# Optimization experiments

Measured on AMD Instinct MI355X. Metric: run time of the kernel, lower is better.

Reference implementation:

```python
import jax, jax.numpy as jnp
import numpy as np

N_NODES = 100000
N_EDGES = 1600000
IN_FEATS = 128
N_HIDDEN = 128
N_CLASSES = 40


def setup_inputs() -> dict:
    key = jax.random.key(0)
    ks = jax.random.split(key, 8)
    features = jax.random.normal(ks[0], (N_NODES, IN_FEATS), dtype=jnp.float32)
    src = jax.random.randint(ks[1], (N_EDGES,), 0, N_NODES, dtype=jnp.int32)
    dst = jax.random.randint(ks[2], (N_EDGES,), 0, N_NODES, dtype=jnp.int32)
    s = 1.0 / np.sqrt(N_HIDDEN)
    W1 = jax.random.normal(ks[3], (IN_FEATS, N_HIDDEN), dtype=jnp.float32) * s
    b1 = jnp.zeros((N_HIDDEN,), dtype=jnp.float32)
    W2 = jax.random.normal(ks[4], (N_HIDDEN, N_HIDDEN), dtype=jnp.float32) * s
    b2 = jnp.zeros((N_HIDDEN,), dtype=jnp.float32)
    W3 = jax.random.normal(ks[5], (N_HIDDEN, N_CLASSES), dtype=jnp.float32) * s
    b3 = jnp.zeros((N_CLASSES,), dtype=jnp.float32)
    return {"features": features, "src": src, "dst": dst,
            "W1": W1, "b1": b1, "W2": W2, "b2": b2, "W3": W3, "b3": b3}


def _gcn_layer(h, src, dst, W, b, activation):
    # message: copy src 'h' along edges; reduce: sum per dst node
    accum = jax.ops.segment_sum(h[src], dst, num_segments=N_NODES)  # [N, d]
    h = accum @ W + b
    if activation:
        h = jax.nn.relu(h)
    return h


def reference(features, src, dst, W1, b1, W2, b2, W3, b3):
    h = _gcn_layer(features, src, dst, W1, b1, True)
    h = _gcn_layer(h, src, dst, W2, b2, True)
    h = _gcn_layer(h, src, dst, W3, b3, False)
    return h  # [N_NODES, N_CLASSES]
```

## Files before the change

kernel.cpp:

```cpp
#include <hip/hip_runtime.h>
#include <hip/hip_bf16.h>


#define PBUCK  800
#define CAPB   4096

typedef __attribute__((ext_vector_type(8))) short short8;
typedef __attribute__((ext_vector_type(4))) float f32x4;

__device__ __forceinline__ float bflo(unsigned u) { return __uint_as_float(u << 16); }
__device__ __forceinline__ float bfhi(unsigned u) { return __uint_as_float(u & 0xffff0000u); }
__device__ __forceinline__ unsigned short f2bf(float f) {
    unsigned u = __float_as_uint(f);
    u = (u + 0x7fffu + ((u >> 16) & 1u)) >> 16;
    return (unsigned short)u;
}
__device__ __forceinline__ unsigned packbf(float a, float b) {
    return (unsigned)f2bf(a) | ((unsigned)f2bf(b) << 16);
}
__device__ __forceinline__ short8 as_short8(uint4 v) {
    union { uint4 u; short8 s; } x; x.u = v; return x.s;
}

__device__ __forceinline__ void packw_body(
    const float* __restrict__ W, unsigned short* __restrict__ Wp, int t)
{
    if (t >= 2048) return;
    int lane = t & 63, cg = (t >> 6) & 7, ks = t >> 9;
    int c = cg * 16 + (lane & 15);
    int kb = ks * 32 + (lane >> 4) * 8;
    unsigned short e[8];
    #pragma unroll
    for (int j = 0; j < 8; ++j) e[j] = f2bf(W[(size_t)(kb + j) * 128 + c]);
    uint4 v = make_uint4((unsigned)e[0] | ((unsigned)e[1] << 16),
                         (unsigned)e[2] | ((unsigned)e[3] << 16),
                         (unsigned)e[4] | ((unsigned)e[5] << 16),
                         (unsigned)e[6] | ((unsigned)e[7] << 16));
    *(uint4*)(Wp + (size_t)t * 8) = v;
}
__device__ __forceinline__ void packw3_body(
    const float* __restrict__ W, unsigned short* __restrict__ Wp, int t)
{
    if (t >= 768) return;
    int lane = t & 63, g = t >> 6;
    int ks = g / 3, cf = g % 3;
    int c = cf * 16 + (lane & 15);
    int kb = ks * 32 + (lane >> 4) * 8;
    unsigned short e[8];
    #pragma unroll
    for (int j = 0; j < 8; ++j)
        e[j] = (c < 40) ? f2bf(W[(size_t)(kb + j) * 40 + c]) : (unsigned short)0;
    uint4 v = make_uint4((unsigned)e[0] | ((unsigned)e[1] << 16),
                         (unsigned)e[2] | ((unsigned)e[3] << 16),
                         (unsigned)e[4] | ((unsigned)e[5] << 16),
                         (unsigned)e[6] | ((unsigned)e[7] << 16));
    *(uint4*)(Wp + (size_t)t * 8) = v;
}

__global__ __launch_bounds__(256) void setup_kernel(
    const float* __restrict__ feat, unsigned short* __restrict__ SC,
    const float* __restrict__ W1, const float* __restrict__ W2,
    const float* __restrict__ W3,
    unsigned short* __restrict__ Wp1, unsigned short* __restrict__ Wp2,
    unsigned short* __restrict__ Wp3, int* __restrict__ pcur,
    int* __restrict__ ghist, int* __restrict__ perm,
    int n_nodes, int castBlocks, int npad)
{
    int b = blockIdx.x, tid = threadIdx.x;
    if (b < castBlocks) {
        int i = b * 256 + tid;
        if (i < n_nodes * 16) {
            const float4* p = (const float4*)(feat + (size_t)i * 8);
            float4 a = p[0], bb = p[1];
            uint4 v = make_uint4(packbf(a.x, a.y), packbf(a.z, a.w),
                                 packbf(bb.x, bb.y), packbf(bb.z, bb.w));
            *(uint4*)(SC + (size_t)i * 8) = v;
        }
        return;
    }
    int r = b - castBlocks;
    if (r < 8)       packw_body(W1, Wp1, r * 256 + tid);
    else if (r < 16) packw_body(W2, Wp2, (r - 8) * 256 + tid);
    else if (r < 19) packw3_body(W3, Wp3, (r - 16) * 256 + tid);
    else if (r < 23) { int i = (r - 19) * 256 + tid; if (i < PBUCK) pcur[i] = i * CAPB; }
    else {
        if (tid < 128) ghist[tid] = 0;
        int idx = n_nodes + tid;
        if (idx < npad) perm[idx] = 0x7fffffff;
    }
}

__global__ __launch_bounds__(1024) void scatter_priv(
    const int* __restrict__ src, const int* __restrict__ dst,
    int* __restrict__ pcur, unsigned* __restrict__ rec, int n_edges)
{
    __shared__ int hist[PBUCK];
    __shared__ int base[PBUCK];
    int nb = gridDim.x;
    int chunk = (n_edges + nb - 1) / nb;
    int lo = blockIdx.x * chunk, hi = min(n_edges, lo + chunk);
    for (int i = threadIdx.x; i < PBUCK; i += 1024) hist[i] = 0;
    __syncthreads();
    for (int e = lo + threadIdx.x; e < hi; e += 1024)
        atomicAdd(&hist[dst[e] >> 7], 1);
    __syncthreads();
    for (int i = threadIdx.x; i < PBUCK; i += 1024) {
        int h = hist[i];
        base[i] = h ? atomicAdd(&pcur[i], h) : 0;
        hist[i] = 0;
    }
    __syncthreads();
    for (int e = lo + threadIdx.x; e < hi; e += 1024) {
        int d = dst[e];
        int b = d >> 7;
        int pos = base[b] + atomicAdd(&hist[b], 1);
        if (pos < (b + 1) * CAPB)
            rec[pos] = (unsigned)src[e] | ((unsigned)(d & 127) << 17);
    }
}

__global__ __launch_bounds__(512) void fill_local3(
    const unsigned* __restrict__ rec, const int* __restrict__ pcur,
    int* __restrict__ offs, int* __restrict__ esrc,
    int* __restrict__ ghist, int n_buckets, int n_nodes)
{
    __shared__ int cnt[128];
    __shared__ int cur[128];
    __shared__ int dh[128];
    __shared__ int wsum[8];
    __shared__ int redA[8], redL[8];
    const int b = blockIdx.x, tid = threadIdx.x;
    const int lane = tid & 63, wid = tid >> 6;

    int accL = 0, accA = 0;
    for (int i = tid; i < n_buckets; i += 512) {
        int t = min(pcur[i] - i * CAPB, CAPB);
        accA += t;
        if (i < b) accL += t;
    }
    #pragma unroll
    for (int off = 32; off; off >>= 1) {
        accA += __shfl_down(accA, off);
        accL += __shfl_down(accL, off);
    }
    if (lane == 0) { redA[wid] = accA; redL[wid] = accL; }
    if (tid < 128) { cnt[tid] = 0; dh[tid] = 0; }
    __syncthreads();
    int baseAll = 0, baseLt = 0;
    #pragma unroll
    for (int w = 0; w < 8; ++w) { baseAll += redA[w]; baseLt += redL[w]; }
    if (b == 0 && tid == 0) offs[n_nodes] = baseAll;

    const int node0 = b << 7;
    const int nN = min(128, n_nodes - node0);
    const int cbeg = b * CAPB;
    const int cend = cbeg + min(pcur[b] - cbeg, CAPB);

    for (int i = cbeg + tid; i < cend; i += 512)
        atomicAdd(&cnt[rec[i] >> 17], 1);
    __syncthreads();

    if (tid < nN) atomicAdd(&dh[min(cnt[tid], 127)], 1);
    int c = (tid < 128) ? cnt[tid] : 0;
    int incl = c;
    #pragma unroll
    for (int off = 1; off < 64; off <<= 1) { int q = __shfl_up(incl, off); if (lane >= off) incl += q; }
    if (lane == 63) wsum[wid] = incl;
    __syncthreads();
    int wpre = 0;
    for (int w = 0; w < wid; ++w) wpre += wsum[w];
    int excl = wpre + incl - c;
    if (tid < nN) { offs[node0 + tid] = baseLt + excl; cur[tid] = excl; }
    if (tid < 128 && dh[tid]) atomicAdd(&ghist[tid], dh[tid]);
    __syncthreads();

    for (int i = cbeg + tid; i < cend; i += 512) {
        unsigned r = rec[i];
        int pos = atomicAdd(&cur[r >> 17], 1);
        esrc[baseLt + pos] = (int)(r & 0x1FFFFu);
    }
}

__global__ __launch_bounds__(128) void deg_scan(
    const int* __restrict__ ghist, int* __restrict__ gcur)
{
    __shared__ int ws[2];
    int tid = threadIdx.x;
    int t = ghist[tid];
    int lane = tid & 63, wid = tid >> 6;
    int incl = t;
    #pragma unroll
    for (int off = 1; off < 64; off <<= 1) { int q = __shfl_up(incl, off); if (lane >= off) incl += q; }
    if (lane == 63) ws[wid] = incl;
    __syncthreads();
    int excl = (wid ? ws[0] : 0) + incl - t;
    gcur[tid] = excl;
}

__global__ __launch_bounds__(256) void deg_place(
    const int* __restrict__ offs, int* __restrict__ gcur,
    int* __restrict__ perm, int n_nodes)
{
    __shared__ int dh[128];
    __shared__ int dbase[128];
    int nb = gridDim.x;
    int chunk = (n_nodes + nb - 1) / nb;
    int lo = blockIdx.x * chunk, hi = min(n_nodes, lo + chunk);
    int tid = threadIdx.x;
    if (tid < 128) dh[tid] = 0;
    __syncthreads();
    for (int n = lo + tid; n < hi; n += 256) {
        int d = min(offs[n + 1] - offs[n], 127);
        atomicAdd(&dh[d], 1);
    }
    __syncthreads();
    if (tid < 128) {
        int h = dh[tid];
        dbase[tid] = h ? atomicAdd(&gcur[tid], h) : 0;
        dh[tid] = 0;
    }
    __syncthreads();
    for (int n = lo + tid; n < hi; n += 256) {
        int d = min(offs[n + 1] - offs[n], 127);
        int pos = dbase[d] + atomicAdd(&dh[d], 1);
        perm[pos] = n;
    }
}

#define GATHER128_BODY(hk, e, end)                                          \
    while (e < end && (e & 3)) {                                            \
        uint4 v = *(const uint4*)(hk + (size_t)esrc[e] * 128);              \
        a0 += bflo(v.x); a1 += bfhi(v.x); a2 += bflo(v.y); a3 += bfhi(v.y); \
        a4 += bflo(v.z); a5 += bfhi(v.z); a6 += bflo(v.w); a7 += bfhi(v.w); \
        ++e;                                                                \
    }                                                                       \
    for (; e + 3 < end; e += 4) {                                           \
        int4 ss = *(const int4*)(esrc + e);                                 \
        uint4 v0 = *(const uint4*)(hk + (size_t)ss.x * 128);                \
        uint4 v1 = *(const uint4*)(hk + (size_t)ss.y * 128);                \
        uint4 v2 = *(const uint4*)(hk + (size_t)ss.z * 128);                \
        uint4 v3 = *(const uint4*)(hk + (size_t)ss.w * 128);                \
        a0 += (bflo(v0.x) + bflo(v1.x)) + (bflo(v2.x) + bflo(v3.x));        \
        a1 += (bfhi(v0.x) + bfhi(v1.x)) + (bfhi(v2.x) + bfhi(v3.x));        \
        a2 += (bflo(v0.y) + bflo(v1.y)) + (bflo(v2.y) + bflo(v3.y));        \
        a3 += (bfhi(v0.y) + bfhi(v1.y)) + (bfhi(v2.y) + bfhi(v3.y));        \
        a4 += (bflo(v0.z) + bflo(v1.z)) + (bflo(v2.z) + bflo(v3.z));        \
        a5 += (bfhi(v0.z) + bfhi(v1.z)) + (bfhi(v2.z) + bfhi(v3.z));        \
        a6 += (bflo(v0.w) + bflo(v1.w)) + (bflo(v2.w) + bflo(v3.w));        \
        a7 += (bfhi(v0.w) + bfhi(v1.w)) + (bfhi(v2.w) + bfhi(v3.w));        \
    }                                                                       \
    for (; e < end; ++e) {                                                  \
        uint4 v = *(const uint4*)(hk + (size_t)esrc[e] * 128);              \
        a0 += bflo(v.x); a1 += bfhi(v.x); a2 += bflo(v.y); a3 += bfhi(v.y); \
        a4 += bflo(v.z); a5 += bfhi(v.z); a6 += bflo(v.w); a7 += bfhi(v.w); \
    }

__global__ __launch_bounds__(256, 8) void gather_gemm_f(
    const unsigned short* __restrict__ h, const int* __restrict__ offs,
    const int* __restrict__ esrc, const int* __restrict__ perm,
    const unsigned short* __restrict__ Wp, const float* __restrict__ bias,
    unsigned short* __restrict__ out, int n_nodes)
{
    __shared__ unsigned short accb[16 * 136];
    const int tid = threadIdx.x;
    const int nl = tid >> 4;
    const int k  = tid & 15;
    const int node0 = blockIdx.x * 16;
    const int node = perm[node0 + nl];

    float a0 = 0.f, a1 = 0.f, a2 = 0.f, a3 = 0.f;
    float a4 = 0.f, a5 = 0.f, a6 = 0.f, a7 = 0.f;
    if (node < n_nodes) {
        const unsigned short* hk = h + k * 8;
        int e = offs[node], end = offs[node + 1];
        GATHER128_BODY(hk, e, end)
    }
    {
        uint4 v = make_uint4(packbf(a0, a1), packbf(a2, a3),
                             packbf(a4, a5), packbf(a6, a7));
        *(uint4*)(accb + nl * 136 + k * 8) = v;
    }
    __syncthreads();

    const int w = tid >> 6, l = tid & 63;
    short8 afr[4];
    #pragma unroll
    for (int ks = 0; ks < 4; ++ks)
        afr[ks] = as_short8(*(const uint4*)(
            accb + (l & 15) * 136 + ks * 32 + (l >> 4) * 8));

    #pragma unroll
    for (int cf = 0; cf < 2; ++cf) {
        int cg = w * 2 + cf;
        int col = cg * 16 + (l & 15);
        float bb = bias[col];
        f32x4 vacc = { bb, bb, bb, bb };
        #pragma unroll
        for (int ks = 0; ks < 4; ++ks) {
            short8 bfr = as_short8(*(const uint4*)(Wp + (size_t)((ks * 8 + cg) * 64 + l) * 8));
            vacc = __builtin_amdgcn_mfma_f32_16x16x32_bf16(afr[ks], bfr, vacc, 0, 0, 0);
        }
        #pragma unroll
        for (int r = 0; r < 4; ++r) {
            int prow = perm[node0 + (l >> 4) * 4 + r];
            if (prow < n_nodes)
                out[(size_t)prow * 128 + col] = f2bf(fmaxf(vacc[r], 0.f));
        }
    }
}

__global__ __launch_bounds__(256, 8) void gather_gemm_ft(
    const unsigned short* __restrict__ h, const int* __restrict__ offs,
    const int* __restrict__ esrc, const int* __restrict__ perm,
    const unsigned short* __restrict__ Wp, const float* __restrict__ bias,
    const unsigned short* __restrict__ Wp3,
    unsigned short* __restrict__ tout, int n_nodes)
{
    __shared__ unsigned short accb[16 * 136];
    const int tid = threadIdx.x;
    const int nl = tid >> 4;
    const int k  = tid & 15;
    const int node0 = blockIdx.x * 16;
    const int node = perm[node0 + nl];

    float a0 = 0.f, a1 = 0.f, a2 = 0.f, a3 = 0.f;
    float a4 = 0.f, a5 = 0.f, a6 = 0.f, a7 = 0.f;
    if (node < n_nodes) {
        const unsigned short* hk = h + k * 8;
        int e = offs[node], end = offs[node + 1];
        GATHER128_BODY(hk, e, end)
    }
    {
        uint4 v = make_uint4(packbf(a0, a1), packbf(a2, a3),
                             packbf(a4, a5), packbf(a6, a7));
        *(uint4*)(accb + nl * 136 + k * 8) = v;
    }
    __syncthreads();

    const int w = tid >> 6, l = tid & 63;
    short8 afr[4];
    #pragma unroll
    for (int ks = 0; ks < 4; ++ks)
        afr[ks] = as_short8(*(const uint4*)(
            accb + (l & 15) * 136 + ks * 32 + (l >> 4) * 8));

    f32x4 hacc[2];
    #pragma unroll
    for (int cf = 0; cf < 2; ++cf) {
        int cg = w * 2 + cf;
        float bb = bias[cg * 16 + (l & 15)];
        f32x4 vacc = { bb, bb, bb, bb };
        #pragma unroll
        for (int ks = 0; ks < 4; ++ks) {
            short8 bfr = as_short8(*(const uint4*)(Wp + (size_t)((ks * 8 + cg) * 64 + l) * 8));
            vacc = __builtin_amdgcn_mfma_f32_16x16x32_bf16(afr[ks], bfr, vacc, 0, 0, 0);
        }
        hacc[cf] = vacc;
    }

    __syncthreads();
    #pragma unroll
    for (int cf = 0; cf < 2; ++cf) {
        int col = (w * 2 + cf) * 16 + (l & 15);
        #pragma unroll
        for (int r = 0; r < 4; ++r)
            accb[((l >> 4) * 4 + r) * 136 + col] = f2bf(fmaxf(hacc[cf][r], 0.f));
    }
    __syncthreads();

    if (w < 3) {
        short8 afr2[4];
        #pragma unroll
        for (int ks = 0; ks < 4; ++ks)
            afr2[ks] = as_short8(*(const uint4*)(
                accb + (l & 15) * 136 + ks * 32 + (l >> 4) * 8));
        f32x4 vacc = { 0.f, 0.f, 0.f, 0.f };
        #pragma unroll
        for (int ks = 0; ks < 4; ++ks) {
            short8 bfr = as_short8(*(const uint4*)(Wp3 + (size_t)((ks * 3 + w) * 64 + l) * 8));
            vacc = __builtin_amdgcn_mfma_f32_16x16x32_bf16(afr2[ks], bfr, vacc, 0, 0, 0);
        }
        int col = w * 16 + (l & 15);
        if (col < 40) {
            #pragma unroll
            for (int r = 0; r < 4; ++r) {
                int prow = perm[node0 + (l >> 4) * 4 + r];
                if (prow < n_nodes)
                    tout[(size_t)prow * 40 + col] = f2bf(vacc[r]);
            }
        }
    }
}

__global__ __launch_bounds__(256) void gather40v(
    const unsigned short* __restrict__ t, const int* __restrict__ offs,
    const int* __restrict__ esrc, const int* __restrict__ perm,
    const float* __restrict__ b3, float* __restrict__ out,
    int n_nodes, int npad)
{
    int lane = threadIdx.x & 63;
    int g = lane / 10;
    int k = lane - g * 10;
    int slot = blockIdx.x * 24 + (threadIdx.x >> 6) * 6 + g;
    if (g >= 6 || slot >= npad) return;
    int node = perm[slot];
    if (node >= n_nodes) return;
    float4 bv = *(const float4*)(b3 + k * 4);
    float a0 = bv.x, a1 = bv.y, a2 = bv.z, a3 = bv.w;
    int e = offs[node], end = offs[node + 1];
    while (e < end && (e & 3)) {
        uint2 v = *(const uint2*)(t + (size_t)esrc[e] * 40 + k * 4);
        a0 += bflo(v.x); a1 += bfhi(v.x); a2 += bflo(v.y); a3 += bfhi(v.y);
        ++e;
    }
    for (; e + 3 < end; e += 4) {
        int4 ss = *(const int4*)(esrc + e);
        uint2 v0 = *(const uint2*)(t + (size_t)ss.x * 40 + k * 4);
        uint2 v1 = *(const uint2*)(t + (size_t)ss.y * 40 + k * 4);
        uint2 v2 = *(const uint2*)(t + (size_t)ss.z * 40 + k * 4);
        uint2 v3 = *(const uint2*)(t + (size_t)ss.w * 40 + k * 4);
        a0 += (bflo(v0.x) + bflo(v1.x)) + (bflo(v2.x) + bflo(v3.x));
        a1 += (bfhi(v0.x) + bfhi(v1.x)) + (bfhi(v2.x) + bfhi(v3.x));
        a2 += (bflo(v0.y) + bflo(v1.y)) + (bflo(v2.y) + bflo(v3.y));
        a3 += (bfhi(v0.y) + bfhi(v1.y)) + (bfhi(v2.y) + bfhi(v3.y));
    }
    for (; e < end; ++e) {
        uint2 v = *(const uint2*)(t + (size_t)esrc[e] * 40 + k * 4);
        a0 += bflo(v.x); a1 += bfhi(v.x); a2 += bflo(v.y); a3 += bfhi(v.y);
    }
    *(float4*)(out + (size_t)node * 40 + k * 4) = make_float4(a0, a1, a2, a3);
}

extern "C" void kernel_launch(void* const* d_in, const int* in_sizes, int n_in,
                              void* d_out, int out_size, void* d_ws, size_t ws_size,
                              hipStream_t stream)
{
    const float* feat = (const float*)d_in[0];
    const int*   src  = (const int*)d_in[1];
    const int*   dst  = (const int*)d_in[2];
    const float* W1   = (const float*)d_in[3];
    const float* b1   = (const float*)d_in[4];
    const float* W2   = (const float*)d_in[5];
    const float* b2   = (const float*)d_in[6];
    const float* W3   = (const float*)d_in[7];
    const float* b3   = (const float*)d_in[8];
    float* out = (float*)d_out;

    const int n_edges = in_sizes[1];
    const int n_nodes = in_sizes[0] / 128;
    const int n_buckets = (n_nodes + 127) >> 7;
    const int fg = (n_nodes + 15) / 16;
    const int npad = fg * 16;

    unsigned short* SC = (unsigned short*)d_ws;
    unsigned short* SD = SC + (size_t)n_nodes * 128;
    unsigned* rec = (unsigned*)(SD + (size_t)n_nodes * 128);
    int*  esrc = (int*)(rec + (size_t)PBUCK * CAPB);
    int*  offs = esrc + n_edges;
    int*  pcur = offs + n_nodes + 1;
    unsigned short* Wp1 = (unsigned short*)(pcur + PBUCK);
    unsigned short* Wp2 = Wp1 + 2048 * 8;
    unsigned short* Wp3 = Wp2 + 2048 * 8;
    int* ghist = (int*)(Wp3 + 768 * 8);
    int* gcur  = ghist + 128;
    int* perm  = gcur + 128;

    const int castBlocks = (n_nodes * 16 + 255) / 256;

    setup_kernel<<<castBlocks + 24, 256, 0, stream>>>(
        feat, SC, W1, W2, W3, Wp1, Wp2, Wp3, pcur, ghist, perm,
        n_nodes, castBlocks, npad);
    scatter_priv<<<512, 1024, 0, stream>>>(src, dst, pcur, rec, n_edges);
    fill_local3<<<n_buckets, 512, 0, stream>>>(rec, pcur, offs, esrc, ghist,
                                               n_buckets, n_nodes);
    deg_scan<<<1, 128, 0, stream>>>(ghist, gcur);
    deg_place<<<256, 256, 0, stream>>>(offs, gcur, perm, n_nodes);

    gather_gemm_f<<<fg, 256, 0, stream>>>(SC, offs, esrc, perm, Wp1, b1, SD, n_nodes);

    gather_gemm_ft<<<fg, 256, 0, stream>>>(SD, offs, esrc, perm, Wp2, b2, Wp3, SC, n_nodes);

    gather40v<<<(npad + 23) / 24, 256, 0, stream>>>(SC, offs, esrc, perm, b3, out,
                                                    n_nodes, npad);
}
```

Before: 246.5 us.

## Drop degree-sorted node permutation and gather nodes in natural order

```diff
diff --git a/kernel.cpp b/kernel.cpp
--- a/kernel.cpp
+++ b/kernel.cpp
@@ -63,8 +63,7 @@
     const float* __restrict__ W3,
     unsigned short* __restrict__ Wp1, unsigned short* __restrict__ Wp2,
     unsigned short* __restrict__ Wp3, int* __restrict__ pcur,
-    int* __restrict__ ghist, int* __restrict__ perm,
-    int n_nodes, int castBlocks, int npad)
+    int n_nodes, int castBlocks)
 {
     int b = blockIdx.x, tid = threadIdx.x;
     if (b < castBlocks) {
@@ -82,12 +81,7 @@
     if (r < 8)       packw_body(W1, Wp1, r * 256 + tid);
     else if (r < 16) packw_body(W2, Wp2, (r - 8) * 256 + tid);
     else if (r < 19) packw3_body(W3, Wp3, (r - 16) * 256 + tid);
-    else if (r < 23) { int i = (r - 19) * 256 + tid; if (i < PBUCK) pcur[i] = i * CAPB; }
-    else {
-        if (tid < 128) ghist[tid] = 0;
-        int idx = n_nodes + tid;
-        if (idx < npad) perm[idx] = 0x7fffffff;
-    }
+    else { int i = (r - 19) * 256 + tid; if (i < PBUCK) pcur[i] = i * CAPB; }
 }
 
 __global__ __launch_bounds__(1024) void scatter_priv(
@@ -122,11 +116,10 @@
 __global__ __launch_bounds__(512) void fill_local3(
     const unsigned* __restrict__ rec, const int* __restrict__ pcur,
     int* __restrict__ offs, int* __restrict__ esrc,
-    int* __restrict__ ghist, int n_buckets, int n_nodes)
+    int n_buckets, int n_nodes)
 {
     __shared__ int cnt[128];
     __shared__ int cur[128];
-    __shared__ int dh[128];
     __shared__ int wsum[8];
     __shared__ int redA[8], redL[8];
     const int b = blockIdx.x, tid = threadIdx.x;
@@ -144,7 +137,7 @@
         accL += __shfl_down(accL, off);
     }
     if (lane == 0) { redA[wid] = accA; redL[wid] = accL; }
-    if (tid < 128) { cnt[tid] = 0; dh[tid] = 0; }
+    if (tid < 128) cnt[tid] = 0;
     __syncthreads();
     int baseAll = 0, baseLt = 0;
     #pragma unroll
@@ -160,7 +153,6 @@
         atomicAdd(&cnt[rec[i] >> 17], 1);
     __syncthreads();
 
-    if (tid < nN) atomicAdd(&dh[min(cnt[tid], 127)], 1);
     int c = (tid < 128) ? cnt[tid] : 0;
     int incl = c;
     #pragma unroll
@@ -171,59 +163,12 @@
     for (int w = 0; w < wid; ++w) wpre += wsum[w];
     int excl = wpre + incl - c;
     if (tid < nN) { offs[node0 + tid] = baseLt + excl; cur[tid] = excl; }
-    if (tid < 128 && dh[tid]) atomicAdd(&ghist[tid], dh[tid]);
     __syncthreads();
 
     for (int i = cbeg + tid; i < cend; i += 512) {
         unsigned r = rec[i];
         int pos = atomicAdd(&cur[r >> 17], 1);
         esrc[baseLt + pos] = (int)(r & 0x1FFFFu);
-    }
-}
-
-__global__ __launch_bounds__(128) void deg_scan(
-    const int* __restrict__ ghist, int* __restrict__ gcur)
-{
-    __shared__ int ws[2];
-    int tid = threadIdx.x;
-    int t = ghist[tid];
-    int lane = tid & 63, wid = tid >> 6;
-    int incl = t;
-    #pragma unroll
-    for (int off = 1; off < 64; off <<= 1) { int q = __shfl_up(incl, off); if (lane >= off) incl += q; }
-    if (lane == 63) ws[wid] = incl;
-    __syncthreads();
-    int excl = (wid ? ws[0] : 0) + incl - t;
-    gcur[tid] = excl;
-}
-
-__global__ __launch_bounds__(256) void deg_place(
-    const int* __restrict__ offs, int* __restrict__ gcur,
-    int* __restrict__ perm, int n_nodes)
-{
-    __shared__ int dh[128];
-    __shared__ int dbase[128];
-    int nb = gridDim.x;
-    int chunk = (n_nodes + nb - 1) / nb;
-    int lo = blockIdx.x * chunk, hi = min(n_nodes, lo + chunk);
-    int tid = threadIdx.x;
-    if (tid < 128) dh[tid] = 0;
-    __syncthreads();
-    for (int n = lo + tid; n < hi; n += 256) {
-        int d = min(offs[n + 1] - offs[n], 127);
-        atomicAdd(&dh[d], 1);
-    }
-    __syncthreads();
-    if (tid < 128) {
-        int h = dh[tid];
-        dbase[tid] = h ? atomicAdd(&gcur[tid], h) : 0;
-        dh[tid] = 0;
-    }
-    __syncthreads();
-    for (int n = lo + tid; n < hi; n += 256) {
-        int d = min(offs[n + 1] - offs[n], 127);
-        int pos = dbase[d] + atomicAdd(&dh[d], 1);
-        perm[pos] = n;
     }
 }
 
@@ -257,16 +202,15 @@
 
 __global__ __launch_bounds__(256, 8) void gather_gemm_f(
     const unsigned short* __restrict__ h, const int* __restrict__ offs,
-    const int* __restrict__ esrc, const int* __restrict__ perm,
-    const unsigned short* __restrict__ Wp, const float* __restrict__ bias,
-    unsigned short* __restrict__ out, int n_nodes)
+    const int* __restrict__ esrc, const unsigned short* __restrict__ Wp,
+    const float* __restrict__ bias, unsigned short* __restrict__ out,
+    int n_nodes)
 {
     __shared__ unsigned short accb[16 * 136];
     const int tid = threadIdx.x;
     const int nl = tid >> 4;
     const int k  = tid & 15;
-    const int node0 = blockIdx.x * 16;
-    const int node = perm[node0 + nl];
+    const int node = blockIdx.x * 16 + nl;
 
     float a0 = 0.f, a1 = 0.f, a2 = 0.f, a3 = 0.f;
     float a4 = 0.f, a5 = 0.f, a6 = 0.f, a7 = 0.f;
@@ -289,6 +233,7 @@
         afr[ks] = as_short8(*(const uint4*)(
             accb + (l & 15) * 136 + ks * 32 + (l >> 4) * 8));
 
+    const int node0 = blockIdx.x * 16;
     #pragma unroll
     for (int cf = 0; cf < 2; ++cf) {
         int cg = w * 2 + cf;
@@ -302,26 +247,24 @@
         }
         #pragma unroll
         for (int r = 0; r < 4; ++r) {
-            int prow = perm[node0 + (l >> 4) * 4 + r];
-            if (prow < n_nodes)
-                out[(size_t)prow * 128 + col] = f2bf(fmaxf(vacc[r], 0.f));
+            int row = node0 + (l >> 4) * 4 + r;
+            if (row < n_nodes)
+                out[(size_t)row * 128 + col] = f2bf(fmaxf(vacc[r], 0.f));
         }
     }
 }
 
 __global__ __launch_bounds__(256, 8) void gather_gemm_ft(
     const unsigned short* __restrict__ h, const int* __restrict__ offs,
-    const int* __restrict__ esrc, const int* __restrict__ perm,
-    const unsigned short* __restrict__ Wp, const float* __restrict__ bias,
-    const unsigned short* __restrict__ Wp3,
+    const int* __restrict__ esrc, const unsigned short* __restrict__ Wp,
+    const float* __restrict__ bias, const unsigned short* __restrict__ Wp3,
     unsigned short* __restrict__ tout, int n_nodes)
 {
     __shared__ unsigned short accb[16 * 136];
     const int tid = threadIdx.x;
     const int nl = tid >> 4;
     const int k  = tid & 15;
-    const int node0 = blockIdx.x * 16;
-    const int node = perm[node0 + nl];
+    const int node = blockIdx.x * 16 + nl;
 
     float a0 = 0.f, a1 = 0.f, a2 = 0.f, a3 = 0.f;
     float a4 = 0.f, a5 = 0.f, a6 = 0.f, a7 = 0.f;
@@ -382,11 +325,12 @@
         }
         int col = w * 16 + (l & 15);
         if (col < 40) {
+            const int node0 = blockIdx.x * 16;
             #pragma unroll
             for (int r = 0; r < 4; ++r) {
-                int prow = perm[node0 + (l >> 4) * 4 + r];
-                if (prow < n_nodes)
-                    tout[(size_t)prow * 40 + col] = f2bf(vacc[r]);
+                int row = node0 + (l >> 4) * 4 + r;
+                if (row < n_nodes)
+                    tout[(size_t)row * 40 + col] = f2bf(vacc[r]);
             }
         }
     }
@@ -394,17 +338,14 @@
 
 __global__ __launch_bounds__(256) void gather40v(
     const unsigned short* __restrict__ t, const int* __restrict__ offs,
-    const int* __restrict__ esrc, const int* __restrict__ perm,
-    const float* __restrict__ b3, float* __restrict__ out,
-    int n_nodes, int npad)
+    const int* __restrict__ esrc, const float* __restrict__ b3,
+    float* __restrict__ out, int n_nodes)
 {
     int lane = threadIdx.x & 63;
     int g = lane / 10;
     int k = lane - g * 10;
-    int slot = blockIdx.x * 24 + (threadIdx.x >> 6) * 6 + g;
-    if (g >= 6 || slot >= npad) return;
-    int node = perm[slot];
-    if (node >= n_nodes) return;
+    int node = blockIdx.x * 24 + (threadIdx.x >> 6) * 6 + g;
+    if (g >= 6 || node >= n_nodes) return;
     float4 bv = *(const float4*)(b3 + k * 4);
     float a0 = bv.x, a1 = bv.y, a2 = bv.z, a3 = bv.w;
     int e = offs[node], end = offs[node + 1];
@@ -450,7 +391,6 @@
     const int n_nodes = in_sizes[0] / 128;
     const int n_buckets = (n_nodes + 127) >> 7;
     const int fg = (n_nodes + 15) / 16;
-    const int npad = fg * 16;
 
     unsigned short* SC = (unsigned short*)d_ws;
     unsigned short* SD = SC + (size_t)n_nodes * 128;
@@ -461,25 +401,18 @@
     unsigned short* Wp1 = (unsigned short*)(pcur + PBUCK);
     unsigned short* Wp2 = Wp1 + 2048 * 8;
     unsigned short* Wp3 = Wp2 + 2048 * 8;
-    int* ghist = (int*)(Wp3 + 768 * 8);
-    int* gcur  = ghist + 128;
-    int* perm  = gcur + 128;
 
     const int castBlocks = (n_nodes * 16 + 255) / 256;
 
-    setup_kernel<<<castBlocks + 24, 256, 0, stream>>>(
-        feat, SC, W1, W2, W3, Wp1, Wp2, Wp3, pcur, ghist, perm,
-        n_nodes, castBlocks, npad);
+    setup_kernel<<<castBlocks + 23, 256, 0, stream>>>(
+        feat, SC, W1, W2, W3, Wp1, Wp2, Wp3, pcur, n_nodes, castBlocks);
     scatter_priv<<<512, 1024, 0, stream>>>(src, dst, pcur, rec, n_edges);
-    fill_local3<<<n_buckets, 512, 0, stream>>>(rec, pcur, offs, esrc, ghist,
+    fill_local3<<<n_buckets, 512, 0, stream>>>(rec, pcur, offs, esrc,
                                                n_buckets, n_nodes);
-    deg_scan<<<1, 128, 0, stream>>>(ghist, gcur);
-    deg_place<<<256, 256, 0, stream>>>(offs, gcur, perm, n_nodes);
-
-    gather_gemm_f<<<fg, 256, 0, stream>>>(SC, offs, esrc, perm, Wp1, b1, SD, n_nodes);
-
-    gather_gemm_ft<<<fg, 256, 0, stream>>>(SD, offs, esrc, perm, Wp2, b2, Wp3, SC, n_nodes);
-
-    gather40v<<<(npad + 23) / 24, 256, 0, stream>>>(SC, offs, esrc, perm, b3, out,
-                                                    n_nodes, npad);
-}
+
+    gather_gemm_f<<<fg, 256, 0, stream>>>(SC, offs, esrc, Wp1, b1, SD, n_nodes);
+
+    gather_gemm_ft<<<fg, 256, 0, stream>>>(SD, offs, esrc, Wp2, b2, Wp3, SC, n_nodes);
+
+    gather40v<<<(n_nodes + 23) / 24, 256, 0, stream>>>(SC, offs, esrc, b3, out, n_nodes);
+}
```

Result: faster. 222.6 us (-9.7%).
